# Performance work log

Hardware: AMD Instinct MI355X
Metric: run time of the kernel (lower is better)

The kernel has to match this reference:

```python
import jax, jax.numpy as jnp
import numpy as np

C = 256  # in_channels
B, N = 8, 2048


def setup_inputs() -> dict:
    key = jax.random.key(0)
    ks = jax.random.split(key, 9)
    s = 1.0 / np.sqrt(C)  # conv1d default init scale (approx)
    return {
        "x": jax.random.normal(ks[0], (B, C, N), jnp.float32),
        "wq": jax.random.normal(ks[1], (C, C), jnp.float32) * s,
        "bq": jax.random.normal(ks[2], (C,), jnp.float32) * s,
        "wk": jax.random.normal(ks[3], (C, C), jnp.float32) * s,
        "bk": jax.random.normal(ks[4], (C,), jnp.float32) * s,
        "wv": jax.random.normal(ks[5], (C, C), jnp.float32) * s,
        "bv": jax.random.normal(ks[6], (C,), jnp.float32) * s,
        "wo": jax.random.normal(ks[7], (C, C), jnp.float32) * s,
        "bo": jax.random.normal(ks[8], (C,), jnp.float32) * s,
    }


def reference(x, wq, bq, wk, bk, wv, bv, wo, bo):
    # 1x1 Conv1d == channel-wise linear: [C_out,C_in] x [B,C_in,N] -> [B,C_out,N]
    proj = lambda w, b, t: jnp.einsum('ci,bin->bcn', w, t) + b[None, :, None]
    q = proj(wq, bq, x)
    k = proj(wk, bk, x)
    v = proj(wv, bv, x)
    norm = 1.0 / (x.shape[1] ** 0.5)
    # scores: w[b,n,m] = sum_c q[b,c,n] k[b,c,m]
    w = jnp.einsum('bcn,bcm->bnm', q, k) * norm
    w = jax.nn.softmax(w, axis=2)
    # attn output: sum_m v[b,c,m] w[b,n,m] -> [B,C,N]
    av = jnp.einsum('bcm,bnm->bcn', v, w)
    out = proj(wo, bo, av)
    return x + out
```

## Files before the change

### kernel.cpp

```cpp
#include <hip/hip_runtime.h>
#include <hip/hip_bf16.h>

#define CCH 256
#define NSEQ 2048
#define BATCH 8

typedef __hip_bfloat16 bf16;
typedef short s8v __attribute__((ext_vector_type(8)));
typedef float f4v __attribute__((ext_vector_type(4)));
typedef float f16v __attribute__((ext_vector_type(16)));

struct __align__(8) bf16x4 { bf16 v[4]; };

__device__ __forceinline__ float b2f(bf16 h) { return __bfloat162float(h); }
__device__ __forceinline__ bf16 f2b(float f) { return __float2bfloat16(f); }

#define MFMA16(a, b, c) __builtin_amdgcn_mfma_f32_16x16x32_bf16((a), (b), (c), 0, 0, 0)
#define MFMA32(a, b, c) __builtin_amdgcn_mfma_f32_32x32x16_bf16((a), (b), (c), 0, 0, 0)

__device__ __forceinline__ void gload_lds16(const bf16* g, bf16* l) {
    __builtin_amdgcn_global_load_lds(
        (const __attribute__((address_space(1))) unsigned int*)(g),
        (__attribute__((address_space(3))) unsigned int*)(l), 16, 0, 0);
}

__global__ __launch_bounds__(256) void prepw_kernel(
    const float* __restrict__ wq, const float* __restrict__ wk,
    const float* __restrict__ wv,
    bf16* __restrict__ wqb, bf16* __restrict__ wkb, bf16* __restrict__ wvb)
{
    int base = (blockIdx.x * 256 + threadIdx.x) * 8;
    int mat = base >> 16, off = base & 65535;
    const float* s = (mat == 0) ? wq : (mat == 1) ? wk : wv;
    bf16* d       = (mat == 0) ? wqb : (mat == 1) ? wkb : wvb;
    #pragma unroll
    for (int j = 0; j < 8; ++j) d[off + j] = f2b(s[off + j]);
}

__global__ __launch_bounds__(256, 2) void qkvprep_kernel(
    const float* __restrict__ x,
    const bf16* __restrict__ Wq, const bf16* __restrict__ Wk,
    const bf16* __restrict__ Wv,
    const float* __restrict__ bq, const float* __restrict__ bk,
    const float* __restrict__ bv,
    bf16* __restrict__ qTt, bf16* __restrict__ kTt, bf16* __restrict__ Vt)
{
    __shared__ bf16 xs[64][260];

    const int tile = blockIdx.x;
    const int flat0 = tile * 64;
    const int phase = blockIdx.y;
    const int b = flat0 >> 11, nn = flat0 & 2047;
    const int tid = threadIdx.x;
    const int w = tid >> 6, lane = tid & 63;
    const int l15 = lane & 15, quad = lane >> 4;
    const float* xb = x + (size_t)b * CCH * NSEQ;

    #pragma unroll
    for (int i = 0; i < 16; ++i) {
        int f4i = i * 256 + tid;
        int c = f4i >> 4, nq = f4i & 15;
        float4 v4 = *(const float4*)&xb[(size_t)c * NSEQ + nn + nq * 4];
        xs[nq * 4 + 0][c] = f2b(v4.x);
        xs[nq * 4 + 1][c] = f2b(v4.y);
        xs[nq * 4 + 2][c] = f2b(v4.z);
        xs[nq * 4 + 3][c] = f2b(v4.w);
    }
    __syncthreads();

    s8v xf[8];
    #pragma unroll
    for (int t = 0; t < 8; ++t)
        xf[t] = *(const s8v*)&xs[w * 16 + l15][t * 32 + quad * 8];

    bf16* qt = qTt + (size_t)tile * 16384;
    bf16* kt = kTt + (size_t)tile * 16384;

    if (phase == 0) {
        #pragma unroll 2
        for (int cs = 0; cs < 16; ++cs) {
            const s8v* wr = (const s8v*)(Wq + (size_t)(cs * 16 + l15) * CCH);
            f4v a = {};
            #pragma unroll
            for (int t = 0; t < 8; ++t) a = MFMA16(xf[t], wr[t * 4 + quad], a);
            int c = cs * 16 + l15;
            float bb = bq[c];
            #pragma unroll
            for (int r = 0; r < 4; ++r) {
                int nl = w * 16 + quad * 4 + r;
                qt[(c >> 3) * 512 + nl * 8 + (c & 7)] = f2b((a[r] + bb) * 0.0625f);
            }
        }
        #pragma unroll 2
        for (int cs = 0; cs < 8; ++cs) {
            const s8v* wr = (const s8v*)(Wk + (size_t)(cs * 16 + l15) * CCH);
            f4v a = {};
            #pragma unroll
            for (int t = 0; t < 8; ++t) a = MFMA16(xf[t], wr[t * 4 + quad], a);
            int c = cs * 16 + l15;
            float bb = bk[c];
            #pragma unroll
            for (int r = 0; r < 4; ++r) {
                int nl = w * 16 + quad * 4 + r;
                kt[(c >> 3) * 512 + nl * 8 + (c & 7)] = f2b(a[r] + bb);
            }
        }
    } else {
        bf16* Vtb = Vt + (size_t)b * CCH * NSEQ;
        const int nb = nn + w * 16 + l15;
        const size_t vbase = (size_t)(nb >> 5) * 8192 + (nb & 31);
        #pragma unroll 2
        for (int cs = 0; cs < 16; ++cs) {
            const s8v* wr = (const s8v*)(Wv + (size_t)(cs * 16 + l15) * CCH);
            f4v a = {};
            #pragma unroll
            for (int t = 0; t < 8; ++t) a = MFMA16(wr[t * 4 + quad], xf[t], a);
            #pragma unroll
            for (int r = 0; r < 4; ++r) {
                int c = cs * 16 + quad * 4 + r;
                Vtb[vbase + (size_t)c * 32] = f2b(a[r] + bv[c]);
            }
        }
        #pragma unroll 2
        for (int cs = 8; cs < 16; ++cs) {
            const s8v* wr = (const s8v*)(Wk + (size_t)(cs * 16 + l15) * CCH);
            f4v a = {};
            #pragma unroll
            for (int t = 0; t < 8; ++t) a = MFMA16(xf[t], wr[t * 4 + quad], a);
            int c = cs * 16 + l15;
            float bb = bk[c];
            #pragma unroll
            for (int r = 0; r < 4; ++r) {
                int nl = w * 16 + quad * 4 + r;
                kt[(c >> 3) * 512 + nl * 8 + (c & 7)] = f2b(a[r] + bb);
            }
        }
    }
}

__global__ __launch_bounds__(256, 2) void flash_kernel(
    const bf16* __restrict__ qTt, const bf16* __restrict__ kTt,
    const bf16* __restrict__ Vt, bf16* __restrict__ Opart,
    float* __restrict__ lpart)
{
    __shared__ bf16 Kc[16384];
    __shared__ bf16 Ps[64][68];
    __shared__ float l_s[2][64];

    const int b = blockIdx.x, nt = blockIdx.y, ms = blockIdx.z;
    const int tid = threadIdx.x;
    const int W = tid >> 6, lane = tid & 63;
    const int l31 = lane & 31, h = lane >> 5;
    const int ng = W >> 1, mg = W & 1;
    const int mb = ms * 16;
    const bf16* Vtb = Vt + (size_t)b * CCH * NSEQ;

    s8v qf[16];
    {
        const bf16* qt = qTt + (size_t)(b * 32 + nt) * 16384;
        #pragma unroll
        for (int t = 0; t < 16; ++t)
            qf[t] = *(const s8v*)&qt[(t * 2 + h) * 512 + (ng * 32 + l31) * 8];
    }
    const bf16* vrow[2];
    #pragma unroll
    for (int cr = 0; cr < 2; ++cr)
        vrow[cr] = Vtb + (size_t)(W * 64 + cr * 32 + l31) * 32 + h * 8;

    f16v O[2][2] = {};
    float lacc[16] = {};

    {
        const bf16* kt = kTt + (size_t)(b * 32 + mb) * 16384;
        #pragma unroll
        for (int i = 0; i < 8; ++i) {
            int ch = W * 8 + i;
            gload_lds16(kt + ch * 512 + lane * 8, &Kc[ch * 512]);
        }
    }
    __syncthreads();

    for (int mt = 0; mt < 16; ++mt) {
        f16v S0 = {}, S1 = {};
        #pragma unroll
        for (int t = 0; t < 8; ++t) {
            s8v kf0 = *(const s8v*)&Kc[(t * 2 + h) * 512 + (mg * 32 + l31) * 8];
            s8v kf1 = *(const s8v*)&Kc[((t + 8) * 2 + h) * 512 + (mg * 32 + l31) * 8];
            S0 = MFMA32(qf[t], kf0, S0);
            S1 = MFMA32(qf[t + 8], kf1, S1);
        }
        s8v vf[2][4];
        #pragma unroll
        for (int ks = 0; ks < 4; ++ks)
            #pragma unroll
            for (int cr = 0; cr < 2; ++cr)
                vf[cr][ks] = *(const s8v*)(vrow[cr]
                    + (size_t)((mb + mt) * 2 + (ks >> 1)) * 8192
                    + (ks & 1) * 16);
        #pragma unroll
        for (int reg = 0; reg < 16; ++reg) {
            float e = __expf(fminf(S0[reg] + S1[reg], 60.f));
            lacc[reg] += e;
            int row = (reg & 3) + 8 * (reg >> 2) + 4 * h;
            Ps[ng * 32 + row][mg * 32 + l31] = f2b(e);
        }
        __syncthreads();

        if (mt < 15) {
            const bf16* kt = kTt + (size_t)(b * 32 + mb + mt + 1) * 16384;
            #pragma unroll
            for (int i = 0; i < 8; ++i) {
                int ch = W * 8 + i;
                gload_lds16(kt + ch * 512 + lane * 8, &Kc[ch * 512]);
            }
        }
        #pragma unroll
        for (int ks = 0; ks < 4; ++ks) {
            s8v pf0 = *(const s8v*)&Ps[l31][ks * 16 + h * 8];
            s8v pf1 = *(const s8v*)&Ps[32 + l31][ks * 16 + h * 8];
            O[0][0] = MFMA32(vf[0][ks], pf0, O[0][0]);
            O[0][1] = MFMA32(vf[0][ks], pf1, O[0][1]);
            O[1][0] = MFMA32(vf[1][ks], pf0, O[1][0]);
            O[1][1] = MFMA32(vf[1][ks], pf1, O[1][1]);
        }
        __syncthreads();
    }

    #pragma unroll
    for (int reg = 0; reg < 16; ++reg) {
        float s = lacc[reg];
        #pragma unroll
        for (int off = 1; off < 32; off <<= 1) s += __shfl_xor(s, off);
        lacc[reg] = s;
    }
    if (l31 == 0) {
        #pragma unroll
        for (int reg = 0; reg < 16; ++reg) {
            int row = (reg & 3) + 8 * (reg >> 2) + 4 * h;
            l_s[mg][ng * 32 + row] = lacc[reg];
        }
    }
    __syncthreads();
    const size_t pb = (size_t)(b * 32 + nt) * 2 + ms;
    if (tid < 64) lpart[pb * 64 + tid] = l_s[0][tid] + l_s[1][tid];

    bf16* Ob = Opart + pb * 16384;
    #pragma unroll
    for (int cr = 0; cr < 2; ++cr)
        #pragma unroll
        for (int g2 = 0; g2 < 2; ++g2) {
            int n = g2 * 32 + l31;
            #pragma unroll
            for (int q2 = 0; q2 < 4; ++q2) {
                bf16x4 pk;
                #pragma unroll
                for (int j = 0; j < 4; ++j) pk.v[j] = f2b(O[cr][g2][q2 * 4 + j]);
                int c = W * 64 + cr * 32 + q2 * 8 + 4 * h;
                *(bf16x4*)&Ob[(size_t)n * 256 + c] = pk;
            }
        }
}

__global__ __launch_bounds__(256, 2) void outproj_kernel(
    const bf16* __restrict__ Opart, const float* __restrict__ lpart,
    const float* __restrict__ Wo, const float* __restrict__ bo,
    const float* __restrict__ x, float* __restrict__ out)
{
    __shared__ bf16 avs[64][260];
    __shared__ float ils[64];

    const int bx = blockIdx.x;
    const int flat0 = bx * 64;
    const int c0 = blockIdx.y * 128;
    const int tid = threadIdx.x;
    const int w = tid >> 6, lane = tid & 63;
    const int l15 = lane & 15, quad = lane >> 4;

    if (tid < 64)
        ils[tid] = 1.f / (lpart[(size_t)(bx * 2) * 64 + tid]
                        + lpart[(size_t)(bx * 2 + 1) * 64 + tid]);
    __syncthreads();

    const bf16x4* O0 = (const bf16x4*)(Opart + (size_t)(bx * 2) * 16384);
    const bf16x4* O1 = O0 + 4096;
    #pragma unroll
    for (int i = 0; i < 16; ++i) {
        int u = i * 256 + tid;
        int n = u >> 6;
        bf16x4 a = O0[u], bb = O1[u];
        float il = ils[n];
        bf16x4 o;
        #pragma unroll
        for (int t = 0; t < 4; ++t)
            o.v[t] = f2b((b2f(a.v[t]) + b2f(bb.v[t])) * il);
        *(bf16x4*)&avs[n][(u & 63) * 4] = o;
    }
    __syncthreads();

    const int bidx = flat0 >> 11, nn = flat0 & 2047;
    const size_t base = (size_t)bidx * CCH * NSEQ;

    for (int g = 0; g < 2; ++g) {
        const int cg = c0 + g * 64 + w * 16;
        s8v af[8];
        #pragma unroll
        for (int t = 0; t < 8; ++t) {
            const float* wp = Wo + (size_t)(cg + l15) * CCH + t * 32 + quad * 8;
            float4 f0 = *(const float4*)wp;
            float4 f1 = *(const float4*)(wp + 4);
            bf16 a8[8] = { f2b(f0.x), f2b(f0.y), f2b(f0.z), f2b(f0.w),
                           f2b(f1.x), f2b(f1.y), f2b(f1.z), f2b(f1.w) };
            af[t] = *(const s8v*)a8;
        }
        f4v O[4] = {};
        #pragma unroll
        for (int nt = 0; nt < 4; ++nt)
            #pragma unroll
            for (int t = 0; t < 8; ++t) {
                s8v br = *(const s8v*)&avs[nt * 16 + l15][t * 32 + quad * 8];
                O[nt] = MFMA16(af[t], br, O[nt]);
            }
        #pragma unroll
        for (int r = 0; r < 4; ++r) {
            int c = cg + quad * 4 + r;
            float bb = bo[c];
            #pragma unroll
            for (int nt = 0; nt < 4; ++nt) {
                size_t idx = base + (size_t)c * NSEQ + nn + nt * 16 + l15;
                out[idx] = O[nt][r] + bb + x[idx];
            }
        }
    }
}

extern "C" void kernel_launch(void* const* d_in, const int* in_sizes, int n_in,
                              void* d_out, int out_size, void* d_ws, size_t ws_size,
                              hipStream_t stream) {
    (void)in_sizes; (void)n_in; (void)out_size; (void)ws_size;
    const float* x  = (const float*)d_in[0];
    const float* wq = (const float*)d_in[1];
    const float* bq = (const float*)d_in[2];
    const float* wk = (const float*)d_in[3];
    const float* bk = (const float*)d_in[4];
    const float* wv = (const float*)d_in[5];
    const float* bv = (const float*)d_in[6];
    const float* wo = (const float*)d_in[7];
    const float* bo = (const float*)d_in[8];
    float* out = (float*)d_out;

    const size_t T = (size_t)BATCH * CCH * NSEQ;
    bf16* qTt  = (bf16*)d_ws;
    bf16* kTt  = qTt + T;
    bf16* Vt   = kTt + T;
    bf16* wqb  = Vt + T;
    bf16* wkb  = wqb + 65536;
    bf16* wvb  = wkb + 65536;
    float* lpart = (float*)(wvb + 65536);
    bf16* Opart  = (bf16*)(lpart + 32768);

    prepw_kernel<<<96, 256, 0, stream>>>(wq, wk, wv, wqb, wkb, wvb);
    qkvprep_kernel<<<dim3(256, 2), 256, 0, stream>>>(
        x, wqb, wkb, wvb, bq, bk, bv, qTt, kTt, Vt);
    flash_kernel<<<dim3(8, 32, 2), 256, 0, stream>>>(qTt, kTt, Vt, Opart, lpart);
    outproj_kernel<<<dim3(256, 2), 256, 0, stream>>>(Opart, lpart, wo, bo, x, out);
}
```

Measured before the change: 190.5 us.

## Stage QKV outputs through LDS, add fragment-major V layout, pre-convert Wo

The QKV projection now writes Q and K tiles into shared memory first and stores them to global as coalesced 16-byte rows instead of scattered 2-byte stores. V is written in a new fragment-major layout, so the flash kernel loads MFMA operands contiguously. The phase-1 work (V plus the second half of K) moves into a separate qkv2 kernel, which adds one launch and reloads x. Wo is converted to bf16 once in prepw, so outproj no longer converts it per block. qkv_kernel still contains a leftover else-branch writing to rsv that is never launched (grid y=1).

```diff
diff --git a/kernel.cpp b/kernel.cpp
--- a/kernel.cpp
+++ b/kernel.cpp
@@ -26,26 +26,28 @@
 
 __global__ __launch_bounds__(256) void prepw_kernel(
     const float* __restrict__ wq, const float* __restrict__ wk,
-    const float* __restrict__ wv,
-    bf16* __restrict__ wqb, bf16* __restrict__ wkb, bf16* __restrict__ wvb)
+    const float* __restrict__ wv, const float* __restrict__ wo,
+    bf16* __restrict__ wqb, bf16* __restrict__ wkb,
+    bf16* __restrict__ wvb, bf16* __restrict__ wob)
 {
     int base = (blockIdx.x * 256 + threadIdx.x) * 8;
     int mat = base >> 16, off = base & 65535;
-    const float* s = (mat == 0) ? wq : (mat == 1) ? wk : wv;
-    bf16* d       = (mat == 0) ? wqb : (mat == 1) ? wkb : wvb;
+    const float* s = (mat == 0) ? wq : (mat == 1) ? wk : (mat == 2) ? wv : wo;
+    bf16* d       = (mat == 0) ? wqb : (mat == 1) ? wkb : (mat == 2) ? wvb : wob;
     #pragma unroll
     for (int j = 0; j < 8; ++j) d[off + j] = f2b(s[off + j]);
 }
 
-__global__ __launch_bounds__(256, 2) void qkvprep_kernel(
+__global__ __launch_bounds__(256, 2) void qkv_kernel(
     const float* __restrict__ x,
     const bf16* __restrict__ Wq, const bf16* __restrict__ Wk,
     const bf16* __restrict__ Wv,
     const float* __restrict__ bq, const float* __restrict__ bk,
     const float* __restrict__ bv,
-    bf16* __restrict__ qTt, bf16* __restrict__ kTt, bf16* __restrict__ Vt)
+    bf16* __restrict__ qTt, bf16* __restrict__ kTt, bf16* __restrict__ Vf)
 {
     __shared__ bf16 xs[64][260];
+    bf16(*rsv)[18] = (bf16(*)[18])&xs[0][0];
 
     const int tile = blockIdx.x;
     const int flat0 = tile * 64;
@@ -72,6 +74,7 @@
     #pragma unroll
     for (int t = 0; t < 8; ++t)
         xf[t] = *(const s8v*)&xs[w * 16 + l15][t * 32 + quad * 8];
+    __syncthreads();
 
     bf16* qt = qTt + (size_t)tile * 16384;
     bf16* kt = kTt + (size_t)tile * 16384;
@@ -86,11 +89,17 @@
             int c = cs * 16 + l15;
             float bb = bq[c];
             #pragma unroll
-            for (int r = 0; r < 4; ++r) {
-                int nl = w * 16 + quad * 4 + r;
-                qt[(c >> 3) * 512 + nl * 8 + (c & 7)] = f2b((a[r] + bb) * 0.0625f);
-            }
-        }
+            for (int r = 0; r < 4; ++r)
+                xs[w * 16 + quad * 4 + r][c] = f2b((a[r] + bb) * 0.0625f);
+        }
+        __syncthreads();
+        #pragma unroll
+        for (int i = 0; i < 8; ++i) {
+            int cblk = w * 8 + i;
+            s8v row = *(const s8v*)&xs[lane][cblk * 8];
+            *(s8v*)&qt[cblk * 512 + lane * 8] = row;
+        }
+        __syncthreads();
         #pragma unroll 2
         for (int cs = 0; cs < 8; ++cs) {
             const s8v* wr = (const s8v*)(Wk + (size_t)(cs * 16 + l15) * CCH);
@@ -100,15 +109,17 @@
             int c = cs * 16 + l15;
             float bb = bk[c];
             #pragma unroll
-            for (int r = 0; r < 4; ++r) {
-                int nl = w * 16 + quad * 4 + r;
-                kt[(c >> 3) * 512 + nl * 8 + (c & 7)] = f2b(a[r] + bb);
-            }
+            for (int r = 0; r < 4; ++r)
+                xs[w * 16 + quad * 4 + r][c] = f2b(a[r] + bb);
+        }
+        __syncthreads();
+        #pragma unroll
+        for (int i = 0; i < 4; ++i) {
+            int cblk = w * 4 + i;
+            s8v row = *(const s8v*)&xs[lane][cblk * 8];
+            *(s8v*)&kt[cblk * 512 + lane * 8] = row;
         }
     } else {
-        bf16* Vtb = Vt + (size_t)b * CCH * NSEQ;
-        const int nb = nn + w * 16 + l15;
-        const size_t vbase = (size_t)(nb >> 5) * 8192 + (nb & 31);
         #pragma unroll 2
         for (int cs = 0; cs < 16; ++cs) {
             const s8v* wr = (const s8v*)(Wv + (size_t)(cs * 16 + l15) * CCH);
@@ -118,29 +129,96 @@
             #pragma unroll
             for (int r = 0; r < 4; ++r) {
                 int c = cs * 16 + quad * 4 + r;
-                Vtb[vbase + (size_t)c * 32] = f2b(a[r] + bv[c]);
+                rsv[c][w * 0 + l15] = f2b(a[r] + bv[c]);
             }
         }
-        #pragma unroll 2
-        for (int cs = 8; cs < 16; ++cs) {
-            const s8v* wr = (const s8v*)(Wk + (size_t)(cs * 16 + l15) * CCH);
-            f4v a = {};
-            #pragma unroll
-            for (int t = 0; t < 8; ++t) a = MFMA16(xf[t], wr[t * 4 + quad], a);
-            int c = cs * 16 + l15;
-            float bb = bk[c];
-            #pragma unroll
-            for (int r = 0; r < 4; ++r) {
-                int nl = w * 16 + quad * 4 + r;
-                kt[(c >> 3) * 512 + nl * 8 + (c & 7)] = f2b(a[r] + bb);
-            }
-        }
+        __syncthreads();
+        __syncthreads();
+    }
+}
+
+
+__global__ __launch_bounds__(256, 2) void qkv2_kernel(
+    const float* __restrict__ x,
+    const bf16* __restrict__ Wk, const bf16* __restrict__ Wv,
+    const float* __restrict__ bk, const float* __restrict__ bv,
+    bf16* __restrict__ kTt, bf16* __restrict__ Vf)
+{
+    __shared__ bf16 xs[64][260];
+    __shared__ bf16 rv[4][256][18];
+
+    const int tile = blockIdx.x;
+    const int flat0 = tile * 64;
+    const int b = flat0 >> 11, nn = flat0 & 2047;
+    const int tid = threadIdx.x;
+    const int w = tid >> 6, lane = tid & 63;
+    const int l15 = lane & 15, quad = lane >> 4;
+    const int l31 = lane & 31, h = lane >> 5;
+    const float* xb = x + (size_t)b * CCH * NSEQ;
+
+    #pragma unroll
+    for (int i = 0; i < 16; ++i) {
+        int f4i = i * 256 + tid;
+        int c = f4i >> 4, nq = f4i & 15;
+        float4 v4 = *(const float4*)&xb[(size_t)c * NSEQ + nn + nq * 4];
+        xs[nq * 4 + 0][c] = f2b(v4.x);
+        xs[nq * 4 + 1][c] = f2b(v4.y);
+        xs[nq * 4 + 2][c] = f2b(v4.z);
+        xs[nq * 4 + 3][c] = f2b(v4.w);
+    }
+    __syncthreads();
+
+    s8v xf[8];
+    #pragma unroll
+    for (int t = 0; t < 8; ++t)
+        xf[t] = *(const s8v*)&xs[w * 16 + l15][t * 32 + quad * 8];
+    __syncthreads();
+
+    #pragma unroll 2
+    for (int cs = 0; cs < 16; ++cs) {
+        const s8v* wr = (const s8v*)(Wv + (size_t)(cs * 16 + l15) * CCH);
+        f4v a = {};
+        #pragma unroll
+        for (int t = 0; t < 8; ++t) a = MFMA16(wr[t * 4 + quad], xf[t], a);
+        #pragma unroll
+        for (int r = 0; r < 4; ++r) {
+            int c = cs * 16 + quad * 4 + r;
+            rv[w][c][l15] = f2b(a[r] + bv[c]);
+        }
+    }
+    #pragma unroll 2
+    for (int cs = 8; cs < 16; ++cs) {
+        const s8v* wr = (const s8v*)(Wk + (size_t)(cs * 16 + l15) * CCH);
+        f4v a = {};
+        #pragma unroll
+        for (int t = 0; t < 8; ++t) a = MFMA16(xf[t], wr[t * 4 + quad], a);
+        int c = cs * 16 + l15;
+        float bb = bk[c];
+        #pragma unroll
+        for (int r = 0; r < 4; ++r)
+            xs[w * 16 + quad * 4 + r][c - 128] = f2b(a[r] + bb);
+    }
+    __syncthreads();
+
+    bf16* Vfb = Vf + (size_t)b * CCH * NSEQ;
+    const int mc = (nn >> 4) + w;
+    #pragma unroll
+    for (int cb = 0; cb < 8; ++cb) {
+        s8v frag = *(const s8v*)&rv[w][cb * 32 + l31][h * 8];
+        *(s8v*)&Vfb[(size_t)(mc * 8 + cb) * 512 + l31 * 16 + h * 8] = frag;
+    }
+    bf16* kt = kTt + (size_t)tile * 16384;
+    #pragma unroll
+    for (int i = 0; i < 4; ++i) {
+        int cblk = w * 4 + i;
+        s8v row = *(const s8v*)&xs[lane][cblk * 8];
+        *(s8v*)&kt[(16 + cblk) * 512 + lane * 8] = row;
     }
 }
 
 __global__ __launch_bounds__(256, 2) void flash_kernel(
     const bf16* __restrict__ qTt, const bf16* __restrict__ kTt,
-    const bf16* __restrict__ Vt, bf16* __restrict__ Opart,
+    const bf16* __restrict__ Vf, bf16* __restrict__ Opart,
     float* __restrict__ lpart)
 {
     __shared__ bf16 Kc[16384];
@@ -153,7 +231,7 @@
     const int l31 = lane & 31, h = lane >> 5;
     const int ng = W >> 1, mg = W & 1;
     const int mb = ms * 16;
-    const bf16* Vtb = Vt + (size_t)b * CCH * NSEQ;
+    const bf16* Vfb = Vf + (size_t)b * CCH * NSEQ;
 
     s8v qf[16];
     {
@@ -162,10 +240,6 @@
         for (int t = 0; t < 16; ++t)
             qf[t] = *(const s8v*)&qt[(t * 2 + h) * 512 + (ng * 32 + l31) * 8];
     }
-    const bf16* vrow[2];
-    #pragma unroll
-    for (int cr = 0; cr < 2; ++cr)
-        vrow[cr] = Vtb + (size_t)(W * 64 + cr * 32 + l31) * 32 + h * 8;
 
     f16v O[2][2] = {};
     float lacc[16] = {};
@@ -191,12 +265,13 @@
         }
         s8v vf[2][4];
         #pragma unroll
-        for (int ks = 0; ks < 4; ++ks)
+        for (int ks = 0; ks < 4; ++ks) {
+            int mc = (mb + mt) * 4 + ks;
             #pragma unroll
             for (int cr = 0; cr < 2; ++cr)
-                vf[cr][ks] = *(const s8v*)(vrow[cr]
-                    + (size_t)((mb + mt) * 2 + (ks >> 1)) * 8192
-                    + (ks & 1) * 16);
+                vf[cr][ks] = *(const s8v*)&Vfb[
+                    (size_t)(mc * 8 + W * 2 + cr) * 512 + l31 * 16 + h * 8];
+        }
         #pragma unroll
         for (int reg = 0; reg < 16; ++reg) {
             float e = __expf(fminf(S0[reg] + S1[reg], 60.f));
@@ -263,7 +338,7 @@
 
 __global__ __launch_bounds__(256, 2) void outproj_kernel(
     const bf16* __restrict__ Opart, const float* __restrict__ lpart,
-    const float* __restrict__ Wo, const float* __restrict__ bo,
+    const bf16* __restrict__ Wob, const float* __restrict__ bo,
     const float* __restrict__ x, float* __restrict__ out)
 {
     __shared__ bf16 avs[64][260];
@@ -302,16 +377,10 @@
 
     for (int g = 0; g < 2; ++g) {
         const int cg = c0 + g * 64 + w * 16;
+        const s8v* Ar = (const s8v*)(Wob + (size_t)(cg + l15) * CCH);
         s8v af[8];
         #pragma unroll
-        for (int t = 0; t < 8; ++t) {
-            const float* wp = Wo + (size_t)(cg + l15) * CCH + t * 32 + quad * 8;
-            float4 f0 = *(const float4*)wp;
-            float4 f1 = *(const float4*)(wp + 4);
-            bf16 a8[8] = { f2b(f0.x), f2b(f0.y), f2b(f0.z), f2b(f0.w),
-                           f2b(f1.x), f2b(f1.y), f2b(f1.z), f2b(f1.w) };
-            af[t] = *(const s8v*)a8;
-        }
+        for (int t = 0; t < 8; ++t) af[t] = Ar[t * 4 + quad];
         f4v O[4] = {};
         #pragma unroll
         for (int nt = 0; nt < 4; ++nt)
@@ -351,16 +420,18 @@
     const size_t T = (size_t)BATCH * CCH * NSEQ;
     bf16* qTt  = (bf16*)d_ws;
     bf16* kTt  = qTt + T;
-    bf16* Vt   = kTt + T;
-    bf16* wqb  = Vt + T;
+    bf16* Vf   = kTt + T;
+    bf16* wqb  = Vf + T;
     bf16* wkb  = wqb + 65536;
     bf16* wvb  = wkb + 65536;
-    float* lpart = (float*)(wvb + 65536);
+    bf16* wob  = wvb + 65536;
+    float* lpart = (float*)(wob + 65536);
     bf16* Opart  = (bf16*)(lpart + 32768);
 
-    prepw_kernel<<<96, 256, 0, stream>>>(wq, wk, wv, wqb, wkb, wvb);
-    qkvprep_kernel<<<dim3(256, 2), 256, 0, stream>>>(
-        x, wqb, wkb, wvb, bq, bk, bv, qTt, kTt, Vt);
-    flash_kernel<<<dim3(8, 32, 2), 256, 0, stream>>>(qTt, kTt, Vt, Opart, lpart);
-    outproj_kernel<<<dim3(256, 2), 256, 0, stream>>>(Opart, lpart, wo, bo, x, out);
-}
+    prepw_kernel<<<128, 256, 0, stream>>>(wq, wk, wv, wo, wqb, wkb, wvb, wob);
+    qkv_kernel<<<dim3(256, 1), 256, 0, stream>>>(
+        x, wqb, wkb, wvb, bq, bk, bv, qTt, kTt, Vf);
+    qkv2_kernel<<<256, 256, 0, stream>>>(x, wkb, wvb, bk, bv, kTt, Vf);
+    flash_kernel<<<dim3(8, 32, 2), 256, 0, stream>>>(qTt, kTt, Vf, Opart, lpart);
+    outproj_kernel<<<dim3(256, 2), 256, 0, stream>>>(Opart, lpart, wob, bo, x, out);
+}
```

Measured after the change: 205.4 us. 1.08x slower.
